# Performance work log

Hardware: AMD Instinct MI355X
Metric: run time of the kernel (lower is better)

The kernel has to match this reference:

```python
import jax, jax.numpy as jnp
import numpy as np

D = 128

def setup_inputs() -> dict:
    key = jax.random.key(0)
    ks = jax.random.split(key, 9)
    B, Nq, Nk = 4, 4096, 4096
    Q = jax.random.normal(ks[0], (B, Nq, D), dtype=jnp.float32)
    K = jax.random.normal(ks[1], (B, Nk, D), dtype=jnp.float32)
    V = jax.random.normal(ks[2], (B, Nk, D), dtype=jnp.float32)
    s = 1.0 / np.sqrt(D)
    Wq = jax.random.normal(ks[3], (D, D), dtype=jnp.float32) * s
    Wk = jax.random.normal(ks[4], (D, D), dtype=jnp.float32) * s
    Wv = jax.random.normal(ks[5], (D, D), dtype=jnp.float32) * s
    bq = jax.random.normal(ks[6], (D,), dtype=jnp.float32) * s
    bk = jax.random.normal(ks[7], (D,), dtype=jnp.float32) * s
    bv = jax.random.normal(ks[8], (D,), dtype=jnp.float32) * s
    return {"Q": Q, "K": K, "V": V, "Wq": Wq, "bq": bq, "Wk": Wk, "bk": bk, "Wv": Wv, "bv": bv}

def reference(Q, K, V, Wq, bq, Wk, bk, Wv, bv):
    scale = jnp.asarray(D ** 0.5, dtype=Q.dtype)
    # torch Linear: x @ W.T + b
    q = jnp.einsum('bnd,ed->bne', Q, Wq) + bq
    k = jnp.einsum('bnd,ed->bne', K, Wk) + bk
    v = jnp.einsum('bnd,ed->bne', V, Wv) + bv
    scores = jnp.einsum('bqe,bke->bqk', q, k) / scale  # [B, Nq, Nk]
    attn = jax.nn.softmax(scores, axis=-1)
    return jnp.einsum('bqk,bke->bqe', attn, v)
```

## Files before the change

kernel.cpp:

```cpp
#include <hip/hip_runtime.h>
#include <math.h>

#define D 128
#define NSPLIT 4

typedef __bf16 v8bf __attribute__((ext_vector_type(8)));
typedef float v4f __attribute__((ext_vector_type(4)));

__device__ inline v8bf load_cvt8(const float* __restrict__ p) {
  const float4* p4 = (const float4*)p;
  float4 a = p4[0], b = p4[1];
  v8bf r;
  r[0] = (__bf16)a.x; r[1] = (__bf16)a.y; r[2] = (__bf16)a.z; r[3] = (__bf16)a.w;
  r[4] = (__bf16)b.x; r[5] = (__bf16)b.y; r[6] = (__bf16)b.z; r[7] = (__bf16)b.w;
  return r;
}

__device__ inline void async_copy16(const void* gsrc, void* ldst) {
  __builtin_amdgcn_global_load_lds(
      (const __attribute__((address_space(1))) void*)gsrc,
      (__attribute__((address_space(3))) void*)ldst, 16, 0, 0);
}


__device__ inline void proj_rowmajor_dev(
    const float* __restrict__ X, const float* __restrict__ W,
    const float* __restrict__ bias, __bf16* __restrict__ Y, float alpha,
    int bx)
{
  const int w = threadIdx.x >> 6, l = threadIdx.x & 63;
  const int l16 = l & 15, l4 = l >> 4;
  const size_t rbase = (size_t)bx * 64 + w * 16;

  v4f acc[8];
  #pragma unroll
  for (int ct = 0; ct < 8; ++ct) acc[ct] = (v4f){0.f, 0.f, 0.f, 0.f};

  #pragma unroll
  for (int kk = 0; kk < 4; ++kk) {
    v8bf a = load_cvt8(X + (rbase + l16) * D + kk * 32 + l4 * 8);
    #pragma unroll
    for (int ct = 0; ct < 8; ++ct) {
      v8bf bw = load_cvt8(W + (size_t)(ct * 16 + l16) * D + kk * 32 + l4 * 8);
      acc[ct] = __builtin_amdgcn_mfma_f32_16x16x32_bf16(a, bw, acc[ct], 0, 0, 0);
    }
  }
  #pragma unroll
  for (int ct = 0; ct < 8; ++ct) {
    float bv = bias[ct * 16 + l16];
    #pragma unroll
    for (int r = 0; r < 4; ++r) {
      float y = (acc[ct][r] + bv) * alpha;
      Y[(rbase + l4 * 4 + r) * D + ct * 16 + l16] = (__bf16)y;
    }
  }
}

__device__ inline void proj_vT_dev(
    const float* __restrict__ X, const float* __restrict__ W,
    const float* __restrict__ bias, __bf16* __restrict__ VT, int Nk,
    int bx)
{
  const int b = bx >> 6;
  const float* Xb = X + (size_t)b * Nk * D;
  __bf16* VTb = VT + (size_t)b * D * Nk;
  const int w = threadIdx.x >> 6, l = threadIdx.x & 63;
  const int l16 = l & 15, l4 = l >> 4;
  const int ebase = w * 32;
  const int nbase = (bx & 63) * 64;

  v4f acc[2][4];
  #pragma unroll
  for (int rt = 0; rt < 2; ++rt)
    #pragma unroll
    for (int ct = 0; ct < 4; ++ct) acc[rt][ct] = (v4f){0.f, 0.f, 0.f, 0.f};

  #pragma unroll
  for (int kk = 0; kk < 4; ++kk) {
    v8bf aw0 = load_cvt8(W + (size_t)(ebase + l16) * D + kk * 32 + l4 * 8);
    v8bf aw1 = load_cvt8(W + (size_t)(ebase + 16 + l16) * D + kk * 32 + l4 * 8);
    #pragma unroll
    for (int ct = 0; ct < 4; ++ct) {
      v8bf bx2 = load_cvt8(Xb + (size_t)(nbase + ct * 16 + l16) * D + kk * 32 + l4 * 8);
      acc[0][ct] = __builtin_amdgcn_mfma_f32_16x16x32_bf16(aw0, bx2, acc[0][ct], 0, 0, 0);
      acc[1][ct] = __builtin_amdgcn_mfma_f32_16x16x32_bf16(aw1, bx2, acc[1][ct], 0, 0, 0);
    }
  }
  #pragma unroll
  for (int rt = 0; rt < 2; ++rt) {
    const int e0 = ebase + rt * 16 + l4 * 4;
    #pragma unroll
    for (int r = 0; r < 4; ++r) {
      float bv = bias[e0 + r];
      #pragma unroll
      for (int ct = 0; ct < 4; ++ct)
        VTb[(size_t)(e0 + r) * Nk + nbase + ct * 16 + l16] = (__bf16)(acc[rt][ct][r] + bv);
    }
  }
}

__global__ __launch_bounds__(256) void proj_all(
    const float* __restrict__ Q, const float* __restrict__ K,
    const float* __restrict__ V,
    const float* __restrict__ Wq, const float* __restrict__ bq,
    const float* __restrict__ Wk, const float* __restrict__ bk,
    const float* __restrict__ Wv, const float* __restrict__ bv,
    __bf16* __restrict__ qbf, __bf16* __restrict__ kbf,
    __bf16* __restrict__ vtbf, int Nk, float alpha)
{
  if (blockIdx.y == 0)       proj_rowmajor_dev(Q, Wq, bq, qbf, alpha, blockIdx.x);
  else if (blockIdx.y == 1)  proj_rowmajor_dev(K, Wk, bk, kbf, 1.0f, blockIdx.x);
  else                       proj_vT_dev(V, Wv, bv, vtbf, Nk, blockIdx.x);
}

__global__ __launch_bounds__(512, 2) void attn_fwd(
    const __bf16* __restrict__ Qb, const __bf16* __restrict__ Kb,
    const __bf16* __restrict__ VTb, float* __restrict__ Out,
    float2* __restrict__ ml, int Nq, int Nk, int NS, int B)
{
  const int nwg = gridDim.x;
  int id = blockIdx.x;
  id = (id & 7) * (nwg >> 3) + (id >> 3);
  const int nx = Nq >> 7;
  const int x = id % nx;
  const int s = (id / nx) % NS;
  const int b = id / (nx * NS);

  const int w = threadIdx.x >> 6, l = threadIdx.x & 63;
  const int l16 = l & 15, l4 = l >> 4;
  const int qbase = x * 128 + w * 16;
  const int chunk = Nk / NS;
  const int kvbeg = s * chunk;
  const int ntiles = chunk >> 6;

  const __bf16* q = Qb + ((size_t)b * Nq + qbase) * D;
  const __bf16* kp = Kb + (size_t)b * Nk * D;
  const __bf16* vt = VTb + (size_t)b * D * Nk;

  __shared__ __align__(16) char k_lds[16384];
  __shared__ __align__(16) char v_lds[16384];
  __shared__ __align__(16) __bf16 p_lds[8][16][72];

  v8bf aq[4];
  #pragma unroll
  for (int kk = 0; kk < 4; ++kk)
    aq[kk] = *(const v8bf*)(q + l16 * D + kk * 32 + l4 * 8);

  v4f accO[8];
  #pragma unroll
  for (int ct = 0; ct < 8; ++ct) accO[ct] = (v4f){0.f, 0.f, 0.f, 0.f};
  float m[4], lsum[4];
  #pragma unroll
  for (int r = 0; r < 4; ++r) { m[r] = -1e30f; lsum[r] = 0.f; }

  for (int t = 0; t < ntiles; ++t) {
    const int kv0 = kvbeg + t * 64;

    {
      const char* kg = (const char*)(kp + (size_t)kv0 * D);
      #pragma unroll
      for (int sweep = 0; sweep < 2; ++sweep) {
        const int flat = sweep * 8192 + w * 1024 + l * 16;
        const int row = flat >> 8;
        const int c = flat & 255;
        const int src = (row << 8) | (c ^ ((row & 7) << 4));
        async_copy16(kg + src, k_lds + sweep * 8192 + w * 1024);
      }
      const char* vg = (const char*)vt + (size_t)kv0 * 2;
      #pragma unroll
      for (int sweep = 0; sweep < 2; ++sweep) {
        const int flat = sweep * 8192 + w * 1024 + l * 16;
        const int row = flat >> 7;
        const int c = flat & 127;
        const int sc = c ^ ((row & 7) << 4);
        async_copy16(vg + (size_t)row * (Nk * 2) + sc,
                     v_lds + sweep * 8192 + w * 1024);
      }
    }
    __syncthreads();

    v4f sc4[4];
    #pragma unroll
    for (int ct = 0; ct < 4; ++ct) sc4[ct] = (v4f){0.f, 0.f, 0.f, 0.f};
    #pragma unroll
    for (int ct = 0; ct < 4; ++ct) {
      const int krow = ct * 16 + l16;
      const int sw = (krow & 7) << 4;
      #pragma unroll
      for (int kk = 0; kk < 4; ++kk) {
        const int cb = kk * 64 + l4 * 16;
        v8bf bk = *(const v8bf*)(k_lds + krow * 256 + (cb ^ sw));
        sc4[ct] = __builtin_amdgcn_mfma_f32_16x16x32_bf16(aq[kk], bk, sc4[ct], 0, 0, 0);
      }
    }

    float lmax[4];
    float g = -1e30f;
    #pragma unroll
    for (int r = 0; r < 4; ++r) {
      lmax[r] = fmaxf(fmaxf(sc4[0][r], sc4[1][r]), fmaxf(sc4[2][r], sc4[3][r]));
      g = fmaxf(g, lmax[r] - m[r]);
    }
    if (__all(g <= 8.0f)) {
      #pragma unroll
      for (int r = 0; r < 4; ++r) {
        float rs = 0.f;
        #pragma unroll
        for (int ct = 0; ct < 4; ++ct) {
          float p = exp2f(sc4[ct][r] - m[r]);
          sc4[ct][r] = p;
          rs += p;
        }
        lsum[r] += rs;
      }
    } else {
      float scale[4];
      #pragma unroll
      for (int r = 0; r < 4; ++r) {
        float mx = lmax[r];
        #pragma unroll
        for (int off = 8; off; off >>= 1) mx = fmaxf(mx, __shfl_xor(mx, off, 64));
        float mn = fmaxf(m[r], mx);
        scale[r] = exp2f(m[r] - mn);
        m[r] = mn;
        float rs = 0.f;
        #pragma unroll
        for (int ct = 0; ct < 4; ++ct) {
          float p = exp2f(sc4[ct][r] - mn);
          sc4[ct][r] = p;
          rs += p;
        }
        lsum[r] = lsum[r] * scale[r] + rs;
      }
      #pragma unroll
      for (int ct = 0; ct < 8; ++ct)
        #pragma unroll
        for (int r = 0; r < 4; ++r) accO[ct][r] *= scale[r];
    }

    #pragma unroll
    for (int ct = 0; ct < 4; ++ct)
      #pragma unroll
      for (int r = 0; r < 4; ++r)
        p_lds[w][l4 * 4 + r][ct * 16 + l16] = (__bf16)sc4[ct][r];

    #pragma unroll
    for (int ks = 0; ks < 2; ++ks) {
      v8bf ap = *(const v8bf*)(&p_lds[w][l16][ks * 32 + l4 * 8]);
      #pragma unroll
      for (int ct = 0; ct < 8; ++ct) {
        const int vrow = ct * 16 + l16;
        const int cb = ks * 64 + l4 * 16;
        v8bf bv = *(const v8bf*)(v_lds + vrow * 128 + (cb ^ ((vrow & 7) << 4)));
        accO[ct] = __builtin_amdgcn_mfma_f32_16x16x32_bf16(ap, bv, accO[ct], 0, 0, 0);
      }
    }
    __syncthreads();
  }

  #pragma unroll
  for (int r = 0; r < 4; ++r) {
    float t2 = lsum[r];
    #pragma unroll
    for (int off = 8; off; off >>= 1) t2 += __shfl_xor(t2, off, 64);
    lsum[r] = t2;
  }

  float* outp = Out + (((size_t)s * B + b) * Nq + qbase) * D;
  if (NS == 1) {
    #pragma unroll
    for (int ct = 0; ct < 8; ++ct)
      #pragma unroll
      for (int r = 0; r < 4; ++r)
        outp[(size_t)(l4 * 4 + r) * D + ct * 16 + l16] = accO[ct][r] / lsum[r];
  } else {
    #pragma unroll
    for (int ct = 0; ct < 8; ++ct)
      #pragma unroll
      for (int r = 0; r < 4; ++r)
        outp[(size_t)(l4 * 4 + r) * D + ct * 16 + l16] = accO[ct][r];
    if (l16 == 0) {
      #pragma unroll
      for (int r = 0; r < 4; ++r) {
        size_t row = (size_t)b * Nq + qbase + l4 * 4 + r;
        ml[(size_t)s * B * Nq + row] = make_float2(m[r], lsum[r]);
      }
    }
  }
}

__global__ __launch_bounds__(256) void attn_combine(
    const float* __restrict__ Opart, const float2* __restrict__ ml,
    float* __restrict__ out, int NS, int rowsTotal)
{
  const int t = threadIdx.x;
  const size_t row = (size_t)blockIdx.x * 2 + (t >> 7);
  const int d = t & 127;

  float mv[NSPLIT], lv[NSPLIT];
  float M = -1e30f;
  #pragma unroll
  for (int s = 0; s < NSPLIT; ++s) {
    float2 x = ml[(size_t)s * rowsTotal + row];
    mv[s] = x.x; lv[s] = x.y;
    M = fmaxf(M, x.x);
  }
  float denom = 0.f, acc = 0.f;
  #pragma unroll
  for (int s = 0; s < NSPLIT; ++s) {
    float wgt = exp2f(mv[s] - M);
    denom += wgt * lv[s];
    acc += wgt * Opart[((size_t)s * rowsTotal + row) * D + d];
  }
  out[row * D + d] = acc / denom;
}

extern "C" void kernel_launch(void* const* d_in, const int* in_sizes, int n_in,
                              void* d_out, int out_size, void* d_ws, size_t ws_size,
                              hipStream_t stream) {
  const float* Q  = (const float*)d_in[0];
  const float* K  = (const float*)d_in[1];
  const float* V  = (const float*)d_in[2];
  const float* Wq = (const float*)d_in[3];
  const float* bq = (const float*)d_in[4];
  const float* Wk = (const float*)d_in[5];
  const float* bk = (const float*)d_in[6];
  const float* Wv = (const float*)d_in[7];
  const float* bv = (const float*)d_in[8];
  float* out = (float*)d_out;

  const int B = 4, Nq = 4096, Nk = 4096;
  const size_t nElems = (size_t)B * Nq * D;
  const size_t bfBytes = nElems * 2;

  char* ws = (char*)d_ws;
  __bf16* qbf  = (__bf16*)(ws);
  __bf16* kbf  = (__bf16*)(ws + bfBytes);
  __bf16* vtbf = (__bf16*)(ws + 2 * bfBytes);
  float*  Opart = (float*)(ws + 3 * bfBytes);
  float2* mlp   = (float2*)(ws + 3 * bfBytes + (size_t)NSPLIT * nElems * 4);

  const size_t needSplit = 3 * bfBytes + (size_t)NSPLIT * nElems * 4 +
                           (size_t)NSPLIT * B * Nq * 8;
  const int NS = (ws_size >= needSplit) ? NSPLIT : 1;

  const float alpha = 1.4426950408889634f / sqrtf((float)D);

  proj_all<<<dim3(B * Nq / 64, 3), 256, 0, stream>>>(
      Q, K, V, Wq, bq, Wk, bk, Wv, bv, qbf, kbf, vtbf, Nk, alpha);

  const int nx = Nq / 128;
  if (NS == 1) {
    attn_fwd<<<dim3(nx * B), 512, 0, stream>>>(
        qbf, kbf, vtbf, out, nullptr, Nq, Nk, 1, B);
  } else {
    attn_fwd<<<dim3(nx * NS * B), 512, 0, stream>>>(
        qbf, kbf, vtbf, Opart, mlp, Nq, Nk, NS, B);
    attn_combine<<<dim3(B * Nq / 2), 256, 0, stream>>>(
        Opart, mlp, out, NS, B * Nq);
  }
}
```

Baseline: 198.2 us.

## Double-buffer K/V tiles in attention and stage projection weights in LDS

The attention loop now uses two K/V LDS buffers and issues the async global-to-LDS copy for the next tile while computing on the current one, so load latency can overlap MFMA work. The projection kernel converts each weight matrix to bf16 once into shared memory instead of every wave reloading and converting it from global memory. The P scratch buffer is re-laid out with an XOR swizzle to reduce LDS bank conflicts. LDS use roughly doubles, which can limit occupancy at two 512-thread blocks per CU. Whether the remaining syncs correctly protect buffer reuse depends on the unseen tail of the loop.

```diff
diff --git a/kernel.cpp b/kernel.cpp
--- a/kernel.cpp
+++ b/kernel.cpp
@@ -20,83 +20,6 @@
   __builtin_amdgcn_global_load_lds(
       (const __attribute__((address_space(1))) void*)gsrc,
       (__attribute__((address_space(3))) void*)ldst, 16, 0, 0);
-}
-
-
-__device__ inline void proj_rowmajor_dev(
-    const float* __restrict__ X, const float* __restrict__ W,
-    const float* __restrict__ bias, __bf16* __restrict__ Y, float alpha,
-    int bx)
-{
-  const int w = threadIdx.x >> 6, l = threadIdx.x & 63;
-  const int l16 = l & 15, l4 = l >> 4;
-  const size_t rbase = (size_t)bx * 64 + w * 16;
-
-  v4f acc[8];
-  #pragma unroll
-  for (int ct = 0; ct < 8; ++ct) acc[ct] = (v4f){0.f, 0.f, 0.f, 0.f};
-
-  #pragma unroll
-  for (int kk = 0; kk < 4; ++kk) {
-    v8bf a = load_cvt8(X + (rbase + l16) * D + kk * 32 + l4 * 8);
-    #pragma unroll
-    for (int ct = 0; ct < 8; ++ct) {
-      v8bf bw = load_cvt8(W + (size_t)(ct * 16 + l16) * D + kk * 32 + l4 * 8);
-      acc[ct] = __builtin_amdgcn_mfma_f32_16x16x32_bf16(a, bw, acc[ct], 0, 0, 0);
-    }
-  }
-  #pragma unroll
-  for (int ct = 0; ct < 8; ++ct) {
-    float bv = bias[ct * 16 + l16];
-    #pragma unroll
-    for (int r = 0; r < 4; ++r) {
-      float y = (acc[ct][r] + bv) * alpha;
-      Y[(rbase + l4 * 4 + r) * D + ct * 16 + l16] = (__bf16)y;
-    }
-  }
-}
-
-__device__ inline void proj_vT_dev(
-    const float* __restrict__ X, const float* __restrict__ W,
-    const float* __restrict__ bias, __bf16* __restrict__ VT, int Nk,
-    int bx)
-{
-  const int b = bx >> 6;
-  const float* Xb = X + (size_t)b * Nk * D;
-  __bf16* VTb = VT + (size_t)b * D * Nk;
-  const int w = threadIdx.x >> 6, l = threadIdx.x & 63;
-  const int l16 = l & 15, l4 = l >> 4;
-  const int ebase = w * 32;
-  const int nbase = (bx & 63) * 64;
-
-  v4f acc[2][4];
-  #pragma unroll
-  for (int rt = 0; rt < 2; ++rt)
-    #pragma unroll
-    for (int ct = 0; ct < 4; ++ct) acc[rt][ct] = (v4f){0.f, 0.f, 0.f, 0.f};
-
-  #pragma unroll
-  for (int kk = 0; kk < 4; ++kk) {
-    v8bf aw0 = load_cvt8(W + (size_t)(ebase + l16) * D + kk * 32 + l4 * 8);
-    v8bf aw1 = load_cvt8(W + (size_t)(ebase + 16 + l16) * D + kk * 32 + l4 * 8);
-    #pragma unroll
-    for (int ct = 0; ct < 4; ++ct) {
-      v8bf bx2 = load_cvt8(Xb + (size_t)(nbase + ct * 16 + l16) * D + kk * 32 + l4 * 8);
-      acc[0][ct] = __builtin_amdgcn_mfma_f32_16x16x32_bf16(aw0, bx2, acc[0][ct], 0, 0, 0);
-      acc[1][ct] = __builtin_amdgcn_mfma_f32_16x16x32_bf16(aw1, bx2, acc[1][ct], 0, 0, 0);
-    }
-  }
-  #pragma unroll
-  for (int rt = 0; rt < 2; ++rt) {
-    const int e0 = ebase + rt * 16 + l4 * 4;
-    #pragma unroll
-    for (int r = 0; r < 4; ++r) {
-      float bv = bias[e0 + r];
-      #pragma unroll
-      for (int ct = 0; ct < 4; ++ct)
-        VTb[(size_t)(e0 + r) * Nk + nbase + ct * 16 + l16] = (__bf16)(acc[rt][ct][r] + bv);
-    }
-  }
 }
 
 __global__ __launch_bounds__(256) void proj_all(
@@ -108,9 +31,91 @@
     __bf16* __restrict__ qbf, __bf16* __restrict__ kbf,
     __bf16* __restrict__ vtbf, int Nk, float alpha)
 {
-  if (blockIdx.y == 0)       proj_rowmajor_dev(Q, Wq, bq, qbf, alpha, blockIdx.x);
-  else if (blockIdx.y == 1)  proj_rowmajor_dev(K, Wk, bk, kbf, 1.0f, blockIdx.x);
-  else                       proj_vT_dev(V, Wv, bv, vtbf, Nk, blockIdx.x);
+  __shared__ __align__(16) __bf16 w_lds[128][136];
+
+  const float* W    = (blockIdx.y == 0) ? Wq : (blockIdx.y == 1) ? Wk : Wv;
+  const float* bias = (blockIdx.y == 0) ? bq : (blockIdx.y == 1) ? bk : bv;
+
+  {
+    const int tid = threadIdx.x;
+    const int r = tid >> 1;
+    const int h = (tid & 1) * 64;
+    #pragma unroll
+    for (int i = 0; i < 8; ++i) {
+      v8bf v = load_cvt8(W + r * D + h + i * 8);
+      *(v8bf*)&w_lds[r][h + i * 8] = v;
+    }
+  }
+  __syncthreads();
+
+  const int w = threadIdx.x >> 6, l = threadIdx.x & 63;
+  const int l16 = l & 15, l4 = l >> 4;
+
+  if (blockIdx.y < 2) {
+    const float* X = (blockIdx.y == 0) ? Q : K;
+    __bf16* Y      = (blockIdx.y == 0) ? qbf : kbf;
+    const float a  = (blockIdx.y == 0) ? alpha : 1.0f;
+    const size_t rbase = (size_t)blockIdx.x * 64 + w * 16;
+
+    v4f acc[8];
+    #pragma unroll
+    for (int ct = 0; ct < 8; ++ct) acc[ct] = (v4f){0.f, 0.f, 0.f, 0.f};
+
+    #pragma unroll
+    for (int kk = 0; kk < 4; ++kk) {
+      v8bf av = load_cvt8(X + (rbase + l16) * D + kk * 32 + l4 * 8);
+      #pragma unroll
+      for (int ct = 0; ct < 8; ++ct) {
+        v8bf bw = *(const v8bf*)&w_lds[ct * 16 + l16][kk * 32 + l4 * 8];
+        acc[ct] = __builtin_amdgcn_mfma_f32_16x16x32_bf16(av, bw, acc[ct], 0, 0, 0);
+      }
+    }
+    #pragma unroll
+    for (int ct = 0; ct < 8; ++ct) {
+      float bv2 = bias[ct * 16 + l16];
+      #pragma unroll
+      for (int r = 0; r < 4; ++r) {
+        float y = (acc[ct][r] + bv2) * a;
+        Y[(rbase + l4 * 4 + r) * D + ct * 16 + l16] = (__bf16)y;
+      }
+    }
+  } else {
+    const int bx = blockIdx.x;
+    const int b = bx >> 6;
+    const float* Xb = V + (size_t)b * Nk * D;
+    __bf16* VTb = vtbf + (size_t)b * D * Nk;
+    const int ebase = w * 32;
+    const int nbase = (bx & 63) * 64;
+
+    v4f acc[2][4];
+    #pragma unroll
+    for (int rt = 0; rt < 2; ++rt)
+      #pragma unroll
+      for (int ct = 0; ct < 4; ++ct) acc[rt][ct] = (v4f){0.f, 0.f, 0.f, 0.f};
+
+    #pragma unroll
+    for (int kk = 0; kk < 4; ++kk) {
+      v8bf aw0 = *(const v8bf*)&w_lds[ebase + l16][kk * 32 + l4 * 8];
+      v8bf aw1 = *(const v8bf*)&w_lds[ebase + 16 + l16][kk * 32 + l4 * 8];
+      #pragma unroll
+      for (int ct = 0; ct < 4; ++ct) {
+        v8bf bx2 = load_cvt8(Xb + (size_t)(nbase + ct * 16 + l16) * D + kk * 32 + l4 * 8);
+        acc[0][ct] = __builtin_amdgcn_mfma_f32_16x16x32_bf16(aw0, bx2, acc[0][ct], 0, 0, 0);
+        acc[1][ct] = __builtin_amdgcn_mfma_f32_16x16x32_bf16(aw1, bx2, acc[1][ct], 0, 0, 0);
+      }
+    }
+    #pragma unroll
+    for (int rt = 0; rt < 2; ++rt) {
+      const int e0 = ebase + rt * 16 + l4 * 4;
+      #pragma unroll
+      for (int r = 0; r < 4; ++r) {
+        float bv2 = bias[e0 + r];
+        #pragma unroll
+        for (int ct = 0; ct < 4; ++ct)
+          VTb[(size_t)(e0 + r) * Nk + nbase + ct * 16 + l16] = (__bf16)(acc[rt][ct][r] + bv2);
+      }
+    }
+  }
 }
 
 __global__ __launch_bounds__(512, 2) void attn_fwd(
@@ -134,12 +139,15 @@
   const int ntiles = chunk >> 6;
 
   const __bf16* q = Qb + ((size_t)b * Nq + qbase) * D;
-  const __bf16* kp = Kb + (size_t)b * Nk * D;
-  const __bf16* vt = VTb + (size_t)b * D * Nk;
-
-  __shared__ __align__(16) char k_lds[16384];
-  __shared__ __align__(16) char v_lds[16384];
-  __shared__ __align__(16) __bf16 p_lds[8][16][72];
+  const char* kg0 = (const char*)(Kb + (size_t)b * Nk * D);
+  const char* vg0 = (const char*)(VTb + (size_t)b * D * Nk);
+
+  __shared__ __align__(16) char k_lds[2][16384];
+  __shared__ __align__(16) char v_lds[2][16384];
+  __shared__ __align__(16) char p_lds[8 * 2048];
+  char* my_p = p_lds + w * 2048;
+
+  const int NkB = Nk * 2;
 
   v8bf aq[4];
   #pragma unroll
@@ -153,31 +161,33 @@
   #pragma unroll
   for (int r = 0; r < 4; ++r) { m[r] = -1e30f; lsum[r] = 0.f; }
 
+  auto stage = [&](int kv0, int buf) {
+    const char* kg = kg0 + (size_t)kv0 * (D * 2);
+    #pragma unroll
+    for (int sweep = 0; sweep < 2; ++sweep) {
+      const int flat = sweep * 8192 + w * 1024 + l * 16;
+      const int row = flat >> 8;
+      const int c = flat & 255;
+      async_copy16(kg + ((row << 8) | (c ^ ((row & 7) << 4))),
+                   &k_lds[buf][sweep * 8192 + w * 1024]);
+    }
+    const char* vg = vg0 + (size_t)kv0 * 2;
+    #pragma unroll
+    for (int sweep = 0; sweep < 2; ++sweep) {
+      const int flat = sweep * 8192 + w * 1024 + l * 16;
+      const int row = flat >> 7;
+      const int c = flat & 127;
+      async_copy16(vg + (size_t)row * NkB + (c ^ ((row & 7) << 4)),
+                   &v_lds[buf][sweep * 8192 + w * 1024]);
+    }
+  };
+
+  stage(kvbeg, 0);
+  __syncthreads();
+
   for (int t = 0; t < ntiles; ++t) {
-    const int kv0 = kvbeg + t * 64;
-
-    {
-      const char* kg = (const char*)(kp + (size_t)kv0 * D);
-      #pragma unroll
-      for (int sweep = 0; sweep < 2; ++sweep) {
-        const int flat = sweep * 8192 + w * 1024 + l * 16;
-        const int row = flat >> 8;
-        const int c = flat & 255;
-        const int src = (row << 8) | (c ^ ((row & 7) << 4));
-        async_copy16(kg + src, k_lds + sweep * 8192 + w * 1024);
-      }
-      const char* vg = (const char*)vt + (size_t)kv0 * 2;
-      #pragma unroll
-      for (int sweep = 0; sweep < 2; ++sweep) {
-        const int flat = sweep * 8192 + w * 1024 + l * 16;
-        const int row = flat >> 7;
-        const int c = flat & 127;
-        const int sc = c ^ ((row & 7) << 4);
-        async_copy16(vg + (size_t)row * (Nk * 2) + sc,
-                     v_lds + sweep * 8192 + w * 1024);
-      }
-    }
-    __syncthreads();
+    const int cur = t & 1;
+    if (t + 1 < ntiles) stage(kvbeg + (t + 1) * 64, cur ^ 1);
 
     v4f sc4[4];
     #pragma unroll
@@ -189,7 +199,7 @@
       #pragma unroll
       for (int kk = 0; kk < 4; ++kk) {
         const int cb = kk * 64 + l4 * 16;
-        v8bf bk = *(const v8bf*)(k_lds + krow * 256 + (cb ^ sw));
+        v8bf bk = *(const v8bf*)(&k_lds[cur][krow * 256 + (cb ^ sw)]);
         sc4[ct] = __builtin_amdgcn_mfma_f32_16x16x32_bf16(aq[kk], bk, sc4[ct], 0, 0, 0);
       }
     }
@@ -241,17 +251,21 @@
     #pragma unroll
     for (int ct = 0; ct < 4; ++ct)
       #pragma unroll
-      for (int r = 0; r < 4; ++r)
-        p_lds[w][l4 * 4 + r][ct * 16 + l16] = (__bf16)sc4[ct][r];
+      for (int r = 0; r < 4; ++r) {
+        const int row = l4 * 4 + r;
+        const int byte = row * 128 + ((ct * 32 + l16 * 2) ^ ((row & 7) << 4));
+        *(__bf16*)(my_p + byte) = (__bf16)sc4[ct][r];
+      }
 
     #pragma unroll
     for (int ks = 0; ks < 2; ++ks) {
-      v8bf ap = *(const v8bf*)(&p_lds[w][l16][ks * 32 + l4 * 8]);
+      const int cbp = ks * 64 + l4 * 16;
+      v8bf ap = *(const v8bf*)(my_p + l16 * 128 + (cbp ^ ((l16 & 7) << 4)));
       #pragma unroll
       for (int ct = 0; ct < 8; ++ct) {
         const int vrow = ct * 16 + l16;
         const int cb = ks * 64 + l4 * 16;
-        v8bf bv = *(const v8bf*)(v_lds + vrow * 128 + (cb ^ ((vrow & 7) << 4)));
+        v8bf bv = *(const v8bf*)(&v_lds[cur][vrow * 128 + (cb ^ ((vrow & 7) << 4))]);
         accO[ct] = __builtin_amdgcn_mfma_f32_16x16x32_bf16(ap, bv, accO[ct], 0, 0, 0);
       }
     }
```

After: 178.5 us. 9.9% less time.
